# Performance work log

Measured on AMD Instinct MI355X. Metric: run time of the kernel, lower is better.

## Reference

```python
import jax, jax.numpy as jnp
import numpy as np

B, S, D, H = 2, 2048, 1024, 16
HS = D // H  # head_size = 64


def setup_inputs() -> dict:
    key = jax.random.key(0)
    k1, k2, k3 = jax.random.split(key, 3)
    x = jax.random.normal(k1, (B, S, D), dtype=jnp.float32)
    c_attn_w = jax.random.normal(k2, (D, 3 * D), dtype=jnp.float32) * (1.0 / np.sqrt(D))
    c_attn_b = jnp.zeros((3 * D,), dtype=jnp.float32)
    c_proj_w = jax.random.normal(k3, (D, D), dtype=jnp.float32) * (1.0 / np.sqrt(D))
    c_proj_b = jnp.zeros((D,), dtype=jnp.float32)
    return {"x": x, "c_attn_w": c_attn_w, "c_attn_b": c_attn_b,
            "c_proj_w": c_proj_w, "c_proj_b": c_proj_b}


def reference(x, c_attn_w, c_attn_b, c_proj_w, c_proj_b):
    b, s, d = x.shape
    qkv = x @ c_attn_w + c_attn_b  # [b, s, 3d]
    q, k, v = jnp.split(qkv, 3, axis=-1)
    # [b, h, s, hs]
    q = q.reshape(b, s, H, HS).transpose(0, 2, 1, 3)
    k = k.reshape(b, s, H, HS).transpose(0, 2, 1, 3)
    v = v.reshape(b, s, H, HS).transpose(0, 2, 1, 3)
    scale = jnp.float32(HS) ** -0.5
    scores = jnp.einsum('bhqd,bhkd->bhqk', q, k) * scale  # [b, h, s, s]
    causal = jnp.tril(jnp.ones((s, s), dtype=bool))
    scores = jnp.where(causal[None, None, :, :], scores, jnp.float32(-jnp.inf))
    weights = jax.nn.softmax(scores, axis=-1)  # attn_dropout p=0 -> identity
    attn = jnp.einsum('bhqk,bhkd->bhqd', weights, v)  # [b, h, s, hs]
    attn = attn.transpose(0, 2, 1, 3).reshape(b, s, d)
    out = attn @ c_proj_w + c_proj_b  # resid_dropout p=0 -> identity
    return out
```

## Files before the change

### kernel.cpp

```cpp
#include <hip/hip_runtime.h>
#include <hip/hip_bf16.h>
#include <stdint.h>

#define TB 2
#define TS 2048
#define TD 1024
#define TH 16
#define THS 64
#define TK 1024

typedef __attribute__((ext_vector_type(8))) short short8;
typedef __attribute__((ext_vector_type(4))) short short4v;
typedef __attribute__((ext_vector_type(4))) float f32x4;
typedef __attribute__((ext_vector_type(16))) float f32x16;
typedef __attribute__((ext_vector_type(4))) unsigned int uint4v;

static __device__ __forceinline__ unsigned short f2bf(float f) {
  union { float f; unsigned u; } v; v.f = f;
  unsigned r = v.u + 0x7FFFu + ((v.u >> 16) & 1u);
  return (unsigned short)(r >> 16);
}

static __device__ __forceinline__ unsigned cvtpk(float a, float b) {
  unsigned r;
  asm("v_cvt_pk_bf16_f32 %0, %1, %2" : "=v"(r) : "v"(a), "v"(b));
  return r;
}

static __device__ __forceinline__ void swap32(unsigned& a, unsigned& b) {
  asm("v_permlane32_swap_b32 %0, %1" : "+v"(a), "+v"(b));
}

static __device__ __forceinline__ void async_copy16(const void* g, void* l) {
  __builtin_amdgcn_global_load_lds(
      (const __attribute__((address_space(1))) unsigned int*)g,
      (__attribute__((address_space(3))) unsigned int*)l, 16, 0, 0);
}

__global__ __launch_bounds__(256) void k_cvt_bf16x4(const float* __restrict__ in,
                                                    ushort4* __restrict__ out, int n4) {
  int i = blockIdx.x * blockDim.x + threadIdx.x;
  if (i >= n4) return;
  float4 v = ((const float4*)in)[i];
  out[i] = make_ushort4(f2bf(v.x), f2bf(v.y), f2bf(v.z), f2bf(v.w));
}

__global__ __launch_bounds__(256) void k_transpose_bf(const float* __restrict__ in,
                                                      unsigned short* __restrict__ out,
                                                      int R, int C) {
  __shared__ float tile[32][33];
  const int tx = threadIdx.x & 31, ty = threadIdx.x >> 5;
  const int r0 = blockIdx.y * 32, c0 = blockIdx.x * 32;
#pragma unroll
  for (int i = 0; i < 32; i += 8)
    tile[ty + i][tx] = in[(size_t)(r0 + ty + i) * C + c0 + tx];
  __syncthreads();
#pragma unroll
  for (int i = 0; i < 32; i += 8)
    out[(size_t)(c0 + ty + i) * R + r0 + tx] = f2bf(tile[tx][ty + i]);
}

__device__ __forceinline__ void gemm_core_k1024(const unsigned short* __restrict__ A,
                                                const unsigned short* __restrict__ BT,
                                                int m0, int n0,
                                                unsigned short* sA, unsigned short* sB,
                                                f32x4 acc[4][4]) {
  const int tid = threadIdx.x;
  const int wave = tid >> 6, lane = tid & 63;
  const int wm = wave >> 1, wn = wave & 1;

  const unsigned short* gsrc = (wave < 2) ? A : BT;
  const int row0 = (wave < 2) ? m0 : n0;
  unsigned short* lbase = (wave < 2) ? sA : sB;
  const int cw = (wave & 1) * 4;
  const size_t gr = (size_t)(row0 + cw * 16 + (lane >> 2)) * TK + (lane & 3) * 8;

#pragma unroll
  for (int mi = 0; mi < 4; ++mi)
#pragma unroll
    for (int ni = 0; ni < 4; ++ni)
      acc[mi][ni] = (f32x4){0.f, 0.f, 0.f, 0.f};

  auto stage = [&](int buf, int kt) {
    const unsigned short* g = gsrc + gr + kt * 32;
    unsigned short* l = lbase + buf * 4096 + cw * 512;
#pragma unroll
    for (int c = 0; c < 4; ++c)
      async_copy16(g + (size_t)c * 16 * TK, l + c * 512);
  };

  stage(0, 0);
  __syncthreads();

  const int l15 = lane & 15, lk8 = (lane >> 4) * 8;
  const int aoff = (wm * 64 + l15) * 32 + lk8;
  const int boff = (wn * 64 + l15) * 32 + lk8;

  for (int kt = 0; kt < TK / 32; ++kt) {
    const int buf = kt & 1;
    if (kt + 1 < TK / 32) stage(buf ^ 1, kt + 1);
    short8 af[4], bfr[4];
#pragma unroll
    for (int i = 0; i < 4; ++i) {
      af[i] = *(const short8*)&sA[buf * 4096 + aoff + i * 16 * 32];
      bfr[i] = *(const short8*)&sB[buf * 4096 + boff + i * 16 * 32];
    }
#pragma unroll
    for (int mi = 0; mi < 4; ++mi)
#pragma unroll
      for (int ni = 0; ni < 4; ++ni)
        acc[mi][ni] = __builtin_amdgcn_mfma_f32_16x16x32_bf16(af[mi], bfr[ni], acc[mi][ni], 0, 0, 0);
    __syncthreads();
  }
}

__global__ __launch_bounds__(256) void k_gemm_qkv(const unsigned short* __restrict__ A,
                                                  const unsigned short* __restrict__ BT,
                                                  const float* __restrict__ bias,
                                                  unsigned short* __restrict__ Qo,
                                                  unsigned short* __restrict__ Ko,
                                                  unsigned short* __restrict__ VTo) {
  __shared__ unsigned short sA[2 * 4096];
  __shared__ unsigned short sB[2 * 4096];
  f32x4 acc[4][4];
  const int m0 = blockIdx.y * 128, n0 = blockIdx.x * 128;
  gemm_core_k1024(A, BT, m0, n0, sA, sB, acc);

  const int lane = threadIdx.x & 63, wave = threadIdx.x >> 6;
  const int wm = wave >> 1, wn = wave & 1;
  const int lr4 = (lane >> 4) * 4, l15 = lane & 15;
#pragma unroll
  for (int mi = 0; mi < 4; ++mi) {
    const int row = m0 + wm * 64 + mi * 16 + lr4;
#pragma unroll
    for (int ni = 0; ni < 4; ++ni) {
      const int col = n0 + wn * 64 + ni * 16 + l15;
      const float bi = bias[col];
      const int reg = col >> 10;
      const int d1 = col & 1023;
      const int h = d1 >> 6, d = d1 & 63;
#pragma unroll
      for (int j = 0; j < 4; ++j) {
        const int t = row + j;
        const int b = t >> 11, s = t & 2047;
        const unsigned short bv = f2bf(acc[mi][ni][j] + bi);
        if (reg == 0)
          Qo[(((size_t)b * TH + h) * TS + s) * THS + d] = bv;
        else if (reg == 1)
          Ko[(((size_t)b * TH + h) * TS + s) * THS + d] = bv;
        else
          VTo[(((size_t)b * TH + h) * THS + d) * TS + s] = bv;
      }
    }
  }
}

__global__ __launch_bounds__(256) void k_attn(const unsigned short* __restrict__ Q,
                                              const unsigned short* __restrict__ K,
                                              const unsigned short* __restrict__ VT,
                                              unsigned short* __restrict__ attn) {
  __shared__ unsigned short sO[4][32 * 68];
  const int lane = threadIdx.x & 63, wave = threadIdx.x >> 6;
  const int l31 = lane & 31, h = lane >> 5;
  int qt = blockIdx.x;
  const int hh = blockIdx.y, b = blockIdx.z;
  if (b) qt = 15 - qt;
  const int qrb = qt * 128 + wave * 32;

  const unsigned short* Qh = Q + (((size_t)b * TH + hh) * TS) * THS;
  const unsigned short* Kh = K + (((size_t)b * TH + hh) * TS) * THS;
  const unsigned short* Vh = VT + (((size_t)b * TH + hh) * THS) * TS;

  short8 qf[4];
#pragma unroll
  for (int c2 = 0; c2 < 4; ++c2)
    qf[c2] = *(const short8*)&Qh[(size_t)(qrb + l31) * THS + c2 * 16 + h * 8];

  f32x16 o0 = {}, o1 = {};
  float m_run = -1e30f, l_run = 0.f;
  const float cl2e = 0.125f * 1.44269504088896340736f;

  const int nkt = (qrb >> 5) + 1;

  short8 kf[4];
#pragma unroll
  for (int c2 = 0; c2 < 4; ++c2)
    kf[c2] = *(const short8*)&Kh[(size_t)l31 * THS + c2 * 16 + h * 8];

  for (int kt = 0; kt < nkt; ++kt) {
    const int kb = kt * 32;
    short8 vf[2][2];
#pragma unroll
    for (int t = 0; t < 2; ++t)
#pragma unroll
      for (int c2 = 0; c2 < 2; ++c2)
        vf[t][c2] = *(const short8*)&Vh[(size_t)(t * 32 + l31) * TS + kb + c2 * 16 + h * 8];

    f32x16 s = {};
#pragma unroll
    for (int c2 = 0; c2 < 4; ++c2)
      s = __builtin_amdgcn_mfma_f32_32x32x16_bf16(kf[c2], qf[c2], s, 0, 0, 0);

    if (kt + 1 < nkt) {
#pragma unroll
      for (int c2 = 0; c2 < 4; ++c2)
        kf[c2] = *(const short8*)&Kh[(size_t)(kb + 32 + l31) * THS + c2 * 16 + h * 8];
    }

    if (kt == nkt - 1) {
#pragma unroll
      for (int r = 0; r < 16; ++r)
        if ((r & 3) + 8 * (r >> 2) + 4 * h > l31) s[r] = -1e30f;
    }

    float tm = s[0];
#pragma unroll
    for (int r = 1; r < 16; ++r) tm = fmaxf(tm, s[r]);
    tm = fmaxf(tm, __shfl_xor(tm, 32));
    const float mn = fmaxf(m_run, tm);
    const float al = __builtin_amdgcn_exp2f((m_run - mn) * cl2e);
    m_run = mn;
    float ts = 0.f;
#pragma unroll
    for (int r = 0; r < 16; ++r) {
      const float p = __builtin_amdgcn_exp2f((s[r] - mn) * cl2e);
      s[r] = p;
      ts += p;
    }
    ts += __shfl_xor(ts, 32);
    l_run = l_run * al + ts;
    o0 *= al;
    o1 *= al;

    unsigned B0 = cvtpk(s[0], s[1]), B1 = cvtpk(s[2], s[3]);
    unsigned B2 = cvtpk(s[4], s[5]), B3 = cvtpk(s[6], s[7]);
    swap32(B0, B2);
    swap32(B1, B3);
    unsigned B4 = cvtpk(s[8], s[9]), B5 = cvtpk(s[10], s[11]);
    unsigned B6 = cvtpk(s[12], s[13]), B7 = cvtpk(s[14], s[15]);
    swap32(B4, B6);
    swap32(B5, B7);
    union U { uint4v u; short8 s8; } u0, u1;
    u0.u = (uint4v){B0, B1, B2, B3};
    u1.u = (uint4v){B4, B5, B6, B7};

    o0 = __builtin_amdgcn_mfma_f32_32x32x16_bf16(vf[0][0], u0.s8, o0, 0, 0, 0);
    o0 = __builtin_amdgcn_mfma_f32_32x32x16_bf16(vf[0][1], u1.s8, o0, 0, 0, 0);
    o1 = __builtin_amdgcn_mfma_f32_32x32x16_bf16(vf[1][0], u0.s8, o1, 0, 0, 0);
    o1 = __builtin_amdgcn_mfma_f32_32x32x16_bf16(vf[1][1], u1.s8, o1, 0, 0, 0);
  }

  const float inv = 1.0f / l_run;
  unsigned* so32 = (unsigned*)&sO[wave][0];
#pragma unroll
  for (int j = 0; j < 8; ++j) {
    const int d0 = ((2 * j) & 3) + 8 * (j >> 1) + 4 * h;
    so32[l31 * 34 + (d0 >> 1)] = cvtpk(o0[2 * j] * inv, o0[2 * j + 1] * inv);
    so32[l31 * 34 + ((32 + d0) >> 1)] = cvtpk(o1[2 * j] * inv, o1[2 * j + 1] * inv);
  }
#pragma unroll
  for (int p2 = 0; p2 < 4; ++p2) {
    const int rp = p2 * 8 + (lane >> 3);
    const int co = (lane & 7) * 8;
    short4v va = *(const short4v*)&sO[wave][rp * 68 + co];
    short4v vb = *(const short4v*)&sO[wave][rp * 68 + co + 4];
    unsigned short* gp = &attn[(size_t)(b * TS + qrb + rp) * TD + hh * THS + co];
    *(short4v*)gp = va;
    *(short4v*)(gp + 4) = vb;
  }
}

__global__ __launch_bounds__(256) void k_gemm_proj(const unsigned short* __restrict__ A,
                                                   const unsigned short* __restrict__ BT,
                                                   const float* __restrict__ bias,
                                                   float* __restrict__ out) {
  __shared__ unsigned short sA[2 * 4096];
  __shared__ unsigned short sB[2 * 4096];
  f32x4 acc[4][4];
  const int m0 = blockIdx.y * 128, n0 = blockIdx.x * 128;
  gemm_core_k1024(A, BT, m0, n0, sA, sB, acc);

  const int lane = threadIdx.x & 63, wave = threadIdx.x >> 6;
  const int wm = wave >> 1, wn = wave & 1;
  const int lr4 = (lane >> 4) * 4, l15 = lane & 15;
#pragma unroll
  for (int mi = 0; mi < 4; ++mi) {
    const int row = m0 + wm * 64 + mi * 16 + lr4;
#pragma unroll
    for (int ni = 0; ni < 4; ++ni) {
      const int col = n0 + wn * 64 + ni * 16 + l15;
      const float bi = bias[col];
#pragma unroll
      for (int j = 0; j < 4; ++j)
        out[(size_t)(row + j) * TD + col] = acc[mi][ni][j] + bi;
    }
  }
}

extern "C" void kernel_launch(void* const* d_in, const int* in_sizes, int n_in,
                              void* d_out, int out_size, void* d_ws, size_t ws_size,
                              hipStream_t stream) {
  const float* x = (const float*)d_in[0];
  const float* c_attn_w = (const float*)d_in[1];
  const float* c_attn_b = (const float*)d_in[2];
  const float* c_proj_w = (const float*)d_in[3];
  const float* c_proj_b = (const float*)d_in[4];
  float* out = (float*)d_out;

  const size_t SZ_XB = (size_t)4096 * 1024 * 2;
  const size_t SZ_WAT = (size_t)3072 * 1024 * 2;
  const size_t SZ_WPT = (size_t)1024 * 1024 * 2;
  const size_t SZ_HEAD = (size_t)TB * TH * TS * THS * 2;
  const size_t SZ_ATT = (size_t)4096 * 1024 * 2;
  if (ws_size < SZ_XB + SZ_WAT + SZ_WPT + 3 * SZ_HEAD + SZ_ATT) return;

  char* ws = (char*)d_ws;
  unsigned short* xb = (unsigned short*)ws;   ws += SZ_XB;
  unsigned short* waT = (unsigned short*)ws;  ws += SZ_WAT;
  unsigned short* wpT = (unsigned short*)ws;  ws += SZ_WPT;
  unsigned short* Qb = (unsigned short*)ws;   ws += SZ_HEAD;
  unsigned short* Kb = (unsigned short*)ws;   ws += SZ_HEAD;
  unsigned short* VTb = (unsigned short*)ws;  ws += SZ_HEAD;
  unsigned short* attn = (unsigned short*)ws; ws += SZ_ATT;

  k_cvt_bf16x4<<<4096, 256, 0, stream>>>(x, (ushort4*)xb, 4096 * 1024 / 4);
  k_transpose_bf<<<dim3(3072 / 32, 1024 / 32), 256, 0, stream>>>(c_attn_w, waT, 1024, 3072);
  k_transpose_bf<<<dim3(1024 / 32, 1024 / 32), 256, 0, stream>>>(c_proj_w, wpT, 1024, 1024);
  k_gemm_qkv<<<dim3(3072 / 128, 4096 / 128), 256, 0, stream>>>(xb, waT, c_attn_b, Qb, Kb, VTb);
  k_attn<<<dim3(TS / 128, TH, TB), 256, 0, stream>>>(Qb, Kb, VTb, attn);
  k_gemm_proj<<<dim3(1024 / 128, 4096 / 128), 256, 0, stream>>>(attn, wpT, c_proj_b, out);
}
```

Measured before the change: 211.2 us.

## Restructure attention into single-wave blocks with XCD-aware scheduling and 64-key tiles

The attention kernel now launches 2048 one-wave blocks instead of 256-thread blocks. Each block's query tile and head are picked from the linear block id so that each XCD works on a fixed set of heads, and long and short causal tiles are interleaved for load balance. The inner loop handles 64 keys per step and prefetches both K and V registers one step ahead. A lazy-rescale threshold skips the max update and the output rescale when the new max does not exceed the running max by much. Risks are higher register pressure from the larger fragments and the correctness reliance on the skip threshold staying numerically safe.

Result: slower. 253.3 us (+20.0%).

```diff
diff --git a/kernel.cpp b/kernel.cpp
--- a/kernel.cpp
+++ b/kernel.cpp
@@ -155,17 +155,21 @@
   }
 }
 
-__global__ __launch_bounds__(256) void k_attn(const unsigned short* __restrict__ Q,
-                                              const unsigned short* __restrict__ K,
-                                              const unsigned short* __restrict__ VT,
-                                              unsigned short* __restrict__ attn) {
-  __shared__ unsigned short sO[4][32 * 68];
-  const int lane = threadIdx.x & 63, wave = threadIdx.x >> 6;
+__global__ __launch_bounds__(64) void k_attn(const unsigned short* __restrict__ Q,
+                                             const unsigned short* __restrict__ K,
+                                             const unsigned short* __restrict__ VT,
+                                             unsigned short* __restrict__ attn) {
+  __shared__ unsigned short sO[32 * 68];
+  const int lane = threadIdx.x;
   const int l31 = lane & 31, h = lane >> 5;
-  int qt = blockIdx.x;
-  const int hh = blockIdx.y, b = blockIdx.z;
-  if (b) qt = 15 - qt;
-  const int qrb = qt * 128 + wave * 32;
+
+  const int lin = blockIdx.x;
+  const int xcd = lin & 7, j = lin >> 3;
+  const int g = j >> 6, jj = j & 63;
+  const int qt = (jj & 1) ? (jj >> 1) : 63 - (jj >> 1);
+  const int pair = xcd * 4 + g;
+  const int b = pair >> 4, hh = pair & 15;
+  const int qrb = qt * 32;
 
   const unsigned short* Qh = Q + (((size_t)b * TH + hh) * TS) * THS;
   const unsigned short* Kh = K + (((size_t)b * TH + hh) * TS) * THS;
@@ -179,91 +183,153 @@
   f32x16 o0 = {}, o1 = {};
   float m_run = -1e30f, l_run = 0.f;
   const float cl2e = 0.125f * 1.44269504088896340736f;
-
-  const int nkt = (qrb >> 5) + 1;
-
-  short8 kf[4];
-#pragma unroll
-  for (int c2 = 0; c2 < 4; ++c2)
-    kf[c2] = *(const short8*)&Kh[(size_t)l31 * THS + c2 * 16 + h * 8];
+  const float THR = 8.0f / cl2e;
+
+  const int nkt = (qrb >> 6) + 1;
+
+  short8 kf[8];
+#pragma unroll
+  for (int t = 0; t < 2; ++t)
+#pragma unroll
+    for (int c2 = 0; c2 < 4; ++c2)
+      kf[t * 4 + c2] = *(const short8*)&Kh[(size_t)(t * 32 + l31) * THS + c2 * 16 + h * 8];
+
+  short8 vf[8];
+#pragma unroll
+  for (int t = 0; t < 2; ++t)
+#pragma unroll
+    for (int c = 0; c < 4; ++c)
+      vf[t * 4 + c] = *(const short8*)&Vh[(size_t)(t * 32 + l31) * TS + c * 16 + h * 8];
 
   for (int kt = 0; kt < nkt; ++kt) {
-    const int kb = kt * 32;
-    short8 vf[2][2];
-#pragma unroll
-    for (int t = 0; t < 2; ++t)
-#pragma unroll
-      for (int c2 = 0; c2 < 2; ++c2)
-        vf[t][c2] = *(const short8*)&Vh[(size_t)(t * 32 + l31) * TS + kb + c2 * 16 + h * 8];
-
-    f32x16 s = {};
+    const int kb = kt * 64;
+    const bool last = (kt == nkt - 1);
+    const bool have2 = (kb + 32) <= (qrb + 31);
+
+    f32x16 s0 = {}, s1 = {};
 #pragma unroll
     for (int c2 = 0; c2 < 4; ++c2)
-      s = __builtin_amdgcn_mfma_f32_32x32x16_bf16(kf[c2], qf[c2], s, 0, 0, 0);
+      s0 = __builtin_amdgcn_mfma_f32_32x32x16_bf16(kf[c2], qf[c2], s0, 0, 0, 0);
+    if (have2) {
+#pragma unroll
+      for (int c2 = 0; c2 < 4; ++c2)
+        s1 = __builtin_amdgcn_mfma_f32_32x32x16_bf16(kf[4 + c2], qf[c2], s1, 0, 0, 0);
+    }
 
     if (kt + 1 < nkt) {
 #pragma unroll
-      for (int c2 = 0; c2 < 4; ++c2)
-        kf[c2] = *(const short8*)&Kh[(size_t)(kb + 32 + l31) * THS + c2 * 16 + h * 8];
-    }
-
-    if (kt == nkt - 1) {
-#pragma unroll
-      for (int r = 0; r < 16; ++r)
-        if ((r & 3) + 8 * (r >> 2) + 4 * h > l31) s[r] = -1e30f;
-    }
-
-    float tm = s[0];
-#pragma unroll
-    for (int r = 1; r < 16; ++r) tm = fmaxf(tm, s[r]);
+      for (int t = 0; t < 2; ++t)
+#pragma unroll
+        for (int c2 = 0; c2 < 4; ++c2)
+          kf[t * 4 + c2] = *(const short8*)&Kh[(size_t)(kb + 64 + t * 32 + l31) * THS + c2 * 16 + h * 8];
+    }
+
+    if (last) {
+      if (kb == qrb) {
+#pragma unroll
+        for (int r = 0; r < 16; ++r)
+          if ((r & 3) + 4 * h + 8 * (r >> 2) > l31) s0[r] = -1e30f;
+      } else {
+#pragma unroll
+        for (int r = 0; r < 16; ++r)
+          if ((r & 3) + 4 * h + 8 * (r >> 2) > l31) s1[r] = -1e30f;
+      }
+    }
+
+    float tm = s0[0];
+#pragma unroll
+    for (int r = 1; r < 16; ++r) tm = fmaxf(tm, s0[r]);
+    if (have2) {
+#pragma unroll
+      for (int r = 0; r < 16; ++r) tm = fmaxf(tm, s1[r]);
+    }
     tm = fmaxf(tm, __shfl_xor(tm, 32));
-    const float mn = fmaxf(m_run, tm);
-    const float al = __builtin_amdgcn_exp2f((m_run - mn) * cl2e);
-    m_run = mn;
+
+    float al;
+    if (__all(tm <= m_run + THR)) {
+      al = 1.0f;
+    } else {
+      const float mn = fmaxf(m_run, tm);
+      al = __builtin_amdgcn_exp2f((m_run - mn) * cl2e);
+      m_run = mn;
+      o0 *= al;
+      o1 *= al;
+    }
     float ts = 0.f;
 #pragma unroll
     for (int r = 0; r < 16; ++r) {
-      const float p = __builtin_amdgcn_exp2f((s[r] - mn) * cl2e);
-      s[r] = p;
+      const float p = __builtin_amdgcn_exp2f((s0[r] - m_run) * cl2e);
+      s0[r] = p;
       ts += p;
+    }
+    if (have2) {
+#pragma unroll
+      for (int r = 0; r < 16; ++r) {
+        const float p = __builtin_amdgcn_exp2f((s1[r] - m_run) * cl2e);
+        s1[r] = p;
+        ts += p;
+      }
     }
     ts += __shfl_xor(ts, 32);
     l_run = l_run * al + ts;
-    o0 *= al;
-    o1 *= al;
-
-    unsigned B0 = cvtpk(s[0], s[1]), B1 = cvtpk(s[2], s[3]);
-    unsigned B2 = cvtpk(s[4], s[5]), B3 = cvtpk(s[6], s[7]);
-    swap32(B0, B2);
-    swap32(B1, B3);
-    unsigned B4 = cvtpk(s[8], s[9]), B5 = cvtpk(s[10], s[11]);
-    unsigned B6 = cvtpk(s[12], s[13]), B7 = cvtpk(s[14], s[15]);
-    swap32(B4, B6);
-    swap32(B5, B7);
-    union U { uint4v u; short8 s8; } u0, u1;
-    u0.u = (uint4v){B0, B1, B2, B3};
-    u1.u = (uint4v){B4, B5, B6, B7};
-
-    o0 = __builtin_amdgcn_mfma_f32_32x32x16_bf16(vf[0][0], u0.s8, o0, 0, 0, 0);
-    o0 = __builtin_amdgcn_mfma_f32_32x32x16_bf16(vf[0][1], u1.s8, o0, 0, 0, 0);
-    o1 = __builtin_amdgcn_mfma_f32_32x32x16_bf16(vf[1][0], u0.s8, o1, 0, 0, 0);
-    o1 = __builtin_amdgcn_mfma_f32_32x32x16_bf16(vf[1][1], u1.s8, o1, 0, 0, 0);
+
+    union U { uint4v u; short8 s8; } u0, u1, u2, u3;
+    {
+      unsigned B0 = cvtpk(s0[0], s0[1]), B1 = cvtpk(s0[2], s0[3]);
+      unsigned B2 = cvtpk(s0[4], s0[5]), B3 = cvtpk(s0[6], s0[7]);
+      swap32(B0, B2);
+      swap32(B1, B3);
+      unsigned B4 = cvtpk(s0[8], s0[9]), B5 = cvtpk(s0[10], s0[11]);
+      unsigned B6 = cvtpk(s0[12], s0[13]), B7 = cvtpk(s0[14], s0[15]);
+      swap32(B4, B6);
+      swap32(B5, B7);
+      u0.u = (uint4v){B0, B1, B2, B3};
+      u1.u = (uint4v){B4, B5, B6, B7};
+    }
+    o0 = __builtin_amdgcn_mfma_f32_32x32x16_bf16(vf[0], u0.s8, o0, 0, 0, 0);
+    o0 = __builtin_amdgcn_mfma_f32_32x32x16_bf16(vf[1], u1.s8, o0, 0, 0, 0);
+    o1 = __builtin_amdgcn_mfma_f32_32x32x16_bf16(vf[4], u0.s8, o1, 0, 0, 0);
+    o1 = __builtin_amdgcn_mfma_f32_32x32x16_bf16(vf[5], u1.s8, o1, 0, 0, 0);
+    if (have2) {
+      unsigned C0 = cvtpk(s1[0], s1[1]), C1 = cvtpk(s1[2], s1[3]);
+      unsigned C2 = cvtpk(s1[4], s1[5]), C3 = cvtpk(s1[6], s1[7]);
+      swap32(C0, C2);
+      swap32(C1, C3);
+      unsigned C4 = cvtpk(s1[8], s1[9]), C5 = cvtpk(s1[10], s1[11]);
+      unsigned C6 = cvtpk(s1[12], s1[13]), C7 = cvtpk(s1[14], s1[15]);
+      swap32(C4, C6);
+      swap32(C5, C7);
+      u2.u = (uint4v){C0, C1, C2, C3};
+      u3.u = (uint4v){C4, C5, C6, C7};
+      o0 = __builtin_amdgcn_mfma_f32_32x32x16_bf16(vf[2], u2.s8, o0, 0, 0, 0);
+      o0 = __builtin_amdgcn_mfma_f32_32x32x16_bf16(vf[3], u3.s8, o0, 0, 0, 0);
+      o1 = __builtin_amdgcn_mfma_f32_32x32x16_bf16(vf[6], u2.s8, o1, 0, 0, 0);
+      o1 = __builtin_amdgcn_mfma_f32_32x32x16_bf16(vf[7], u3.s8, o1, 0, 0, 0);
+    }
+
+    if (kt + 1 < nkt) {
+#pragma unroll
+      for (int t = 0; t < 2; ++t)
+#pragma unroll
+        for (int c = 0; c < 4; ++c)
+          vf[t * 4 + c] = *(const short8*)&Vh[(size_t)(t * 32 + l31) * TS + kb + 64 + c * 16 + h * 8];
+    }
   }
 
   const float inv = 1.0f / l_run;
-  unsigned* so32 = (unsigned*)&sO[wave][0];
-#pragma unroll
-  for (int j = 0; j < 8; ++j) {
-    const int d0 = ((2 * j) & 3) + 8 * (j >> 1) + 4 * h;
-    so32[l31 * 34 + (d0 >> 1)] = cvtpk(o0[2 * j] * inv, o0[2 * j + 1] * inv);
-    so32[l31 * 34 + ((32 + d0) >> 1)] = cvtpk(o1[2 * j] * inv, o1[2 * j + 1] * inv);
+  unsigned* so32 = (unsigned*)&sO[0];
+#pragma unroll
+  for (int j2 = 0; j2 < 8; ++j2) {
+    const int d0 = ((2 * j2) & 3) + 8 * (j2 >> 1) + 4 * h;
+    so32[l31 * 34 + (d0 >> 1)] = cvtpk(o0[2 * j2] * inv, o0[2 * j2 + 1] * inv);
+    so32[l31 * 34 + ((32 + d0) >> 1)] = cvtpk(o1[2 * j2] * inv, o1[2 * j2 + 1] * inv);
   }
 #pragma unroll
   for (int p2 = 0; p2 < 4; ++p2) {
     const int rp = p2 * 8 + (lane >> 3);
     const int co = (lane & 7) * 8;
-    short4v va = *(const short4v*)&sO[wave][rp * 68 + co];
-    short4v vb = *(const short4v*)&sO[wave][rp * 68 + co + 4];
+    short4v va = *(const short4v*)&sO[rp * 68 + co];
+    short4v vb = *(const short4v*)&sO[rp * 68 + co + 4];
     unsigned short* gp = &attn[(size_t)(b * TS + qrb + rp) * TD + hh * THS + co];
     *(short4v*)gp = va;
     *(short4v*)(gp + 4) = vb;
@@ -327,6 +393,6 @@
   k_transpose_bf<<<dim3(3072 / 32, 1024 / 32), 256, 0, stream>>>(c_attn_w, waT, 1024, 3072);
   k_transpose_bf<<<dim3(1024 / 32, 1024 / 32), 256, 0, stream>>>(c_proj_w, wpT, 1024, 1024);
   k_gemm_qkv<<<dim3(3072 / 128, 4096 / 128), 256, 0, stream>>>(xb, waT, c_attn_b, Qb, Kb, VTb);
-  k_attn<<<dim3(TS / 128, TH, TB), 256, 0, stream>>>(Qb, Kb, VTb, attn);
+  k_attn<<<dim3(2048), 64, 0, stream>>>(Qb, Kb, VTb, attn);
   k_gemm_proj<<<dim3(1024 / 128, 4096 / 128), 256, 0, stream>>>(attn, wpT, c_proj_b, out);
 }
```

## Remap attention blocks per XCD, add lazy softmax rescale and MFMA priority

Applied to the files above, without the earlier changes.

Flattens the attention grid to 1D and maps blocks so that each XCD handles a fixed set of (batch, head) pairs, with causal tiles interleaved long/short for better L2 locality and load balance. It adds a conditional online-softmax rescale that is skipped when the new max stays within a threshold of the running max, avoiding the accumulator multiplies. It also raises wave priority around the MFMA sections and tree-reduces the max and sum. The threshold trick lets exponents grow up to 2^8 before rescaling, which is safe in fp32 but adds a wave-wide vote.

New measurement: 262.5 us. 24.3% more time.

```diff
diff --git a/kernel.cpp b/kernel.cpp
--- a/kernel.cpp
+++ b/kernel.cpp
@@ -162,9 +162,13 @@
   __shared__ unsigned short sO[4][32 * 68];
   const int lane = threadIdx.x & 63, wave = threadIdx.x >> 6;
   const int l31 = lane & 31, h = lane >> 5;
-  int qt = blockIdx.x;
-  const int hh = blockIdx.y, b = blockIdx.z;
-  if (b) qt = 15 - qt;
+
+  const int lin = blockIdx.x;
+  const int xcd = lin & 7, j = lin >> 3;
+  const int g = j >> 4, jt = j & 15;
+  const int pair = xcd * 4 + g;
+  const int b = pair >> 4, hh = pair & 15;
+  const int qt = (jt & 1) ? (jt >> 1) : 15 - (jt >> 1);
   const int qrb = qt * 128 + wave * 32;
 
   const unsigned short* Qh = Q + (((size_t)b * TH + hh) * TS) * THS;
@@ -179,6 +183,7 @@
   f32x16 o0 = {}, o1 = {};
   float m_run = -1e30f, l_run = 0.f;
   const float cl2e = 0.125f * 1.44269504088896340736f;
+  const float THR = 8.0f / cl2e;
 
   const int nkt = (qrb >> 5) + 1;
 
@@ -197,9 +202,11 @@
         vf[t][c2] = *(const short8*)&Vh[(size_t)(t * 32 + l31) * TS + kb + c2 * 16 + h * 8];
 
     f32x16 s = {};
+    __builtin_amdgcn_s_setprio(1);
 #pragma unroll
     for (int c2 = 0; c2 < 4; ++c2)
       s = __builtin_amdgcn_mfma_f32_32x32x16_bf16(kf[c2], qf[c2], s, 0, 0, 0);
+    __builtin_amdgcn_s_setprio(0);
 
     if (kt + 1 < nkt) {
 #pragma unroll
@@ -213,24 +220,33 @@
         if ((r & 3) + 8 * (r >> 2) + 4 * h > l31) s[r] = -1e30f;
     }
 
-    float tm = s[0];
-#pragma unroll
-    for (int r = 1; r < 16; ++r) tm = fmaxf(tm, s[r]);
+    const float ma = fmaxf(fmaxf(s[0], s[1]), fmaxf(s[2], s[3]));
+    const float mb = fmaxf(fmaxf(s[4], s[5]), fmaxf(s[6], s[7]));
+    const float mc = fmaxf(fmaxf(s[8], s[9]), fmaxf(s[10], s[11]));
+    const float md = fmaxf(fmaxf(s[12], s[13]), fmaxf(s[14], s[15]));
+    float tm = fmaxf(fmaxf(ma, mb), fmaxf(mc, md));
     tm = fmaxf(tm, __shfl_xor(tm, 32));
-    const float mn = fmaxf(m_run, tm);
-    const float al = __builtin_amdgcn_exp2f((m_run - mn) * cl2e);
-    m_run = mn;
-    float ts = 0.f;
-#pragma unroll
-    for (int r = 0; r < 16; ++r) {
-      const float p = __builtin_amdgcn_exp2f((s[r] - mn) * cl2e);
-      s[r] = p;
-      ts += p;
-    }
+
+    float al;
+    if (__all(tm <= m_run + THR)) {
+      al = 1.0f;
+    } else {
+      const float mn = fmaxf(m_run, tm);
+      al = __builtin_amdgcn_exp2f((m_run - mn) * cl2e);
+      m_run = mn;
+      o0 *= al;
+      o1 *= al;
+    }
+#pragma unroll
+    for (int r = 0; r < 16; ++r)
+      s[r] = __builtin_amdgcn_exp2f((s[r] - m_run) * cl2e);
+    const float sa = (s[0] + s[1]) + (s[2] + s[3]);
+    const float sb2 = (s[4] + s[5]) + (s[6] + s[7]);
+    const float sc = (s[8] + s[9]) + (s[10] + s[11]);
+    const float sd = (s[12] + s[13]) + (s[14] + s[15]);
+    float ts = (sa + sb2) + (sc + sd);
     ts += __shfl_xor(ts, 32);
     l_run = l_run * al + ts;
-    o0 *= al;
-    o1 *= al;
 
     unsigned B0 = cvtpk(s[0], s[1]), B1 = cvtpk(s[2], s[3]);
     unsigned B2 = cvtpk(s[4], s[5]), B3 = cvtpk(s[6], s[7]);
@@ -244,19 +260,21 @@
     u0.u = (uint4v){B0, B1, B2, B3};
     u1.u = (uint4v){B4, B5, B6, B7};
 
+    __builtin_amdgcn_s_setprio(1);
     o0 = __builtin_amdgcn_mfma_f32_32x32x16_bf16(vf[0][0], u0.s8, o0, 0, 0, 0);
     o0 = __builtin_amdgcn_mfma_f32_32x32x16_bf16(vf[0][1], u1.s8, o0, 0, 0, 0);
     o1 = __builtin_amdgcn_mfma_f32_32x32x16_bf16(vf[1][0], u0.s8, o1, 0, 0, 0);
     o1 = __builtin_amdgcn_mfma_f32_32x32x16_bf16(vf[1][1], u1.s8, o1, 0, 0, 0);
+    __builtin_amdgcn_s_setprio(0);
   }
 
   const float inv = 1.0f / l_run;
   unsigned* so32 = (unsigned*)&sO[wave][0];
 #pragma unroll
-  for (int j = 0; j < 8; ++j) {
-    const int d0 = ((2 * j) & 3) + 8 * (j >> 1) + 4 * h;
-    so32[l31 * 34 + (d0 >> 1)] = cvtpk(o0[2 * j] * inv, o0[2 * j + 1] * inv);
-    so32[l31 * 34 + ((32 + d0) >> 1)] = cvtpk(o1[2 * j] * inv, o1[2 * j + 1] * inv);
+  for (int j2 = 0; j2 < 8; ++j2) {
+    const int d0 = ((2 * j2) & 3) + 8 * (j2 >> 1) + 4 * h;
+    so32[l31 * 34 + (d0 >> 1)] = cvtpk(o0[2 * j2] * inv, o0[2 * j2 + 1] * inv);
+    so32[l31 * 34 + ((32 + d0) >> 1)] = cvtpk(o1[2 * j2] * inv, o1[2 * j2 + 1] * inv);
   }
 #pragma unroll
   for (int p2 = 0; p2 < 4; ++p2) {
@@ -327,6 +345,6 @@
   k_transpose_bf<<<dim3(3072 / 32, 1024 / 32), 256, 0, stream>>>(c_attn_w, waT, 1024, 3072);
   k_transpose_bf<<<dim3(1024 / 32, 1024 / 32), 256, 0, stream>>>(c_proj_w, wpT, 1024, 1024);
   k_gemm_qkv<<<dim3(3072 / 128, 4096 / 128), 256, 0, stream>>>(xb, waT, c_attn_b, Qb, Kb, VTb);
-  k_attn<<<dim3(TS / 128, TH, TB), 256, 0, stream>>>(Qb, Kb, VTb, attn);
+  k_attn<<<dim3(512), 256, 0, stream>>>(Qb, Kb, VTb, attn);
   k_gemm_proj<<<dim3(1024 / 128, 4096 / 128), 256, 0, stream>>>(attn, wpT, c_proj_b, out);
 }
```
